# Kernel optimization log

Measured on AMD Instinct MI355X. Metric: run time of the kernel, lower is better.

The kernel has to match this reference:

```python
import jax, jax.numpy as jnp
import numpy as np

RADIUS = 4  # matches init radius


def _bilinear_sample(v, grid):
    """Faithful F.grid_sample(v, grid, mode='bilinear', align_corners=True, padding_mode='zeros').
    v: (B,C,H,W); grid: (B,Hg,Wg,2) in [-1,1]; grid[...,0]->width(x), grid[...,1]->height(y)."""
    B, C, H, W = v.shape
    Hg, Wg = grid.shape[1], grid.shape[2]
    ix = (grid[..., 0] + 1.0) * 0.5 * (W - 1)
    iy = (grid[..., 1] + 1.0) * 0.5 * (H - 1)
    x0 = jnp.floor(ix); y0 = jnp.floor(iy)
    x1 = x0 + 1.0;      y1 = y0 + 1.0
    wx1 = ix - x0; wx0 = 1.0 - wx1
    wy1 = iy - y0; wy0 = 1.0 - wy1
    v_flat = v.reshape(B, C, H * W)
    out = jnp.zeros((B, C, Hg, Wg), v.dtype)
    for xf, yf, w in ((x0, y0, wx0 * wy0), (x1, y0, wx1 * wy0),
                      (x0, y1, wx0 * wy1), (x1, y1, wx1 * wy1)):
        valid = (xf >= 0) & (xf <= W - 1) & (yf >= 0) & (yf <= H - 1)
        xi = jnp.clip(xf, 0, W - 1).astype(jnp.int32)
        yi = jnp.clip(yf, 0, H - 1).astype(jnp.int32)
        idx = (yi * W + xi).reshape(B, 1, Hg * Wg)
        g = jnp.take_along_axis(v_flat, idx, axis=2).reshape(B, C, Hg, Wg)
        out = out + g * (w * valid)[:, None, :, :]
    return out


def setup_inputs() -> dict:
    key = jax.random.key(0)
    ks = jax.random.split(key, 5)
    B, C, H, W, K = 4, 128, 128, 128, 8
    x = jax.random.normal(ks[0], (B, C, H, W), jnp.float32)
    psf_tbl = jax.random.randint(ks[1], (B, H, W, K, 2), 0, 128)  # absolute pixel anchors
    delta = jax.random.normal(ks[2], (1, 1, 1, K, 2), jnp.float32) * 0.1
    w_qkv = jax.random.normal(ks[3], (3 * C, C), jnp.float32) * (C ** -0.5)  # 1x1 conv, no bias
    w_proj = jax.random.normal(ks[4], (C, C), jnp.float32) * (C ** -0.5)
    return {"x": x, "psf_tbl": psf_tbl, "delta": delta, "w_qkv": w_qkv, "w_proj": w_proj}


def reference(x, psf_tbl, delta, w_qkv, w_proj):
    B, C, H, W = x.shape
    K = psf_tbl.shape[3]
    qkv = jnp.einsum('oc,bchw->bohw', w_qkv, x)  # 1x1 conv to_qkv
    q, k, v = jnp.split(qkv, 3, axis=1)
    offsets = psf_tbl.astype(x.dtype) + jnp.tanh(delta) * RADIUS  # (B,H,W,K,2)
    norm = jnp.array([H - 1, W - 1], x.dtype)
    grid = (offsets / norm * 2.0 - 1.0).reshape(B, H, W * K, 2)
    k_s = _bilinear_sample(k, grid).reshape(B, C, H, W, K)
    v_s = _bilinear_sample(v, grid).reshape(B, C, H, W, K)
    attn = jnp.einsum('bchw,bchwk->bhwk', q, k_s) * (C ** -0.5)
    attn = jax.nn.softmax(attn, axis=-1)  # softmax over K sampled points
    out = jnp.einsum('bhwk,bchwk->bchw', attn, v_s)
    return x + jnp.einsum('oc,bchw->bohw', w_proj, out)
```

## Files before the change

### kernel.cpp

```cpp
#include <hip/hip_runtime.h>

#define HW 16384
#define C 128

typedef __attribute__((ext_vector_type(8))) short short8;
typedef __attribute__((ext_vector_type(4))) float f32x4;
typedef __attribute__((ext_vector_type(2))) float f32x2;
typedef __attribute__((ext_vector_type(16))) int v16i;

__device__ __forceinline__ unsigned short f2bf(float f) {
  union { float f; unsigned u; } v; v.f = f;
  return (unsigned short)((v.u + 0x7fffu + ((v.u >> 16) & 1u)) >> 16);
}
#if __has_builtin(__builtin_amdgcn_cvt_pk_bf16_f32)
typedef __attribute__((ext_vector_type(2))) __bf16 bf16x2;
__device__ __forceinline__ unsigned pk2(float a, float b) {
  union { bf16x2 v; unsigned u; } cv;
  cv.v = __builtin_amdgcn_cvt_pk_bf16_f32(a, b);
  return cv.u;
}
#else
__device__ __forceinline__ unsigned pk2(float a, float b) {
  return (unsigned)f2bf(a) | ((unsigned)f2bf(b) << 16);
}
#endif
__device__ __forceinline__ unsigned short f2bf1(float a) {
  return (unsigned short)(pk2(a, a) & 0xffffu);
}
__device__ __forceinline__ float bflo(unsigned w) {
  union { unsigned u; float f; } v; v.u = w << 16; return v.f;
}
__device__ __forceinline__ float bfhi(unsigned w) {
  union { unsigned u; float f; } v; v.u = w & 0xffff0000u; return v.f;
}
__device__ __forceinline__ float asf(int u) {
  union { int u; float f; } v; v.u = u; return v.f;
}
__device__ __forceinline__ float bf2f(unsigned short h) {
  union { unsigned u; float f; } v; v.u = ((unsigned)h) << 16; return v.f;
}

__global__ __launch_bounds__(128) void k_prep(const float* __restrict__ w_qkv,
                                              const float* __restrict__ w_proj,
                                              const float* __restrict__ delta,
                                              unsigned short* __restrict__ Mt,
                                              unsigned short* __restrict__ Pm,
                                              float* __restrict__ pw,
                                              int* __restrict__ pi) {
  const int bid = blockIdx.x;
  const int t = threadIdx.x;
  if (bid == 256) {
    if (t < 8) {
      float s0 = tanhf(delta[t * 2 + 0]) * 4.0f;
      float s1 = tanhf(delta[t * 2 + 1]) * 4.0f;
      float f0 = floorf(s0), f1 = floorf(s1);
      pi[2 * t + 0] = (int)f0;
      pi[2 * t + 1] = (int)f1;
      float fx = s0 - f0, fy = s1 - f1;
      pw[4 * t + 0] = (1.0f - fx) * (1.0f - fy);
      pw[4 * t + 1] = fx * (1.0f - fy);
      pw[4 * t + 2] = (1.0f - fx) * fy;
      pw[4 * t + 3] = fx * fy;
    }
    return;
  }
  const int R = bid & 127;
  float acc = 0.0f;
  if (bid < 128) {
    const float* wq = w_qkv;
    const float* wk = w_qkv + 128 * 128;
    #pragma unroll 16
    for (int j = 0; j < 128; ++j)
      acc += wk[j * 128 + R] * wq[j * 128 + t];
    acc *= 0.08838834764831845f;
    Mt[R * 128 + (t ^ ((R & 7) << 3))] = f2bf1(acc);
  } else {
    const float* wv = w_qkv + 2 * 128 * 128;
    const float* wp = w_proj + (size_t)R * 128;
    #pragma unroll 16
    for (int j = 0; j < 128; ++j)
      acc += wp[j] * wv[j * 128 + t];
    Pm[R * 128 + (t ^ ((R & 7) << 3))] = f2bf1(acc);
  }
}

__global__ __launch_bounds__(256) void k_qx(const float* __restrict__ x,
                                            const unsigned short* __restrict__ Mt,
                                            unsigned short* __restrict__ qb,
                                            unsigned* __restrict__ xq) {
  __shared__ __align__(16) unsigned char smem[65536];
  unsigned short* Xs = (unsigned short*)smem;
  unsigned short* Ws = (unsigned short*)(smem + 32768);
  const int t = threadIdx.x;
  const int gpix0 = blockIdx.x * 128;
  const int b = gpix0 >> 14;
  const int hw0 = gpix0 & (HW - 1);

  const float* xb = x + (size_t)b * C * HW + hw0;
  #pragma unroll
  for (int i = 0; i < 16; ++i) {
    int linear = i * 256 + t;
    int p = linear & 127;
    int c4 = (linear >> 7) * 4;
    float a0 = xb[(size_t)(c4 + 0) * HW + p];
    float a1 = xb[(size_t)(c4 + 1) * HW + p];
    float a2 = xb[(size_t)(c4 + 2) * HW + p];
    float a3 = xb[(size_t)(c4 + 3) * HW + p];
    int cc = c4 ^ ((p & 7) << 3);
    *(uint2*)&Xs[p * 128 + cc] = make_uint2(pk2(a0, a1), pk2(a2, a3));
  }
  #pragma unroll
  for (int i = 0; i < 8; ++i)
    ((uint4*)Ws)[i * 256 + t] = ((const uint4*)Mt)[i * 256 + t];
  __syncthreads();

  #pragma unroll
  for (int i = 0; i < 8; ++i) {
    int linear = i * 256 + t;
    int c8 = (linear & 15) * 8;
    int prow = linear >> 4;
    uint4 v = *(const uint4*)&Xs[prow * 128 + (c8 ^ ((prow & 7) << 3))];
    *(uint4*)&xq[((size_t)(gpix0 + prow)) * 64 + (c8 >> 1)] = v;
  }

  const int wave = t >> 6, lane = t & 63;
  const int wr = wave >> 1, wc = wave & 1;
  const int rsel = lane & 15, quad = lane >> 4;

  f32x4 acc[4][4];
  #pragma unroll
  for (int mi = 0; mi < 4; ++mi)
    #pragma unroll
    for (int ni = 0; ni < 4; ++ni) acc[mi][ni] = (f32x4){0.f, 0.f, 0.f, 0.f};
  #pragma unroll
  for (int ks = 0; ks < 4; ++ks) {
    const int koff = ks * 32 + quad * 8;
    short8 afr[4], bfr[4];
    #pragma unroll
    for (int mi = 0; mi < 4; ++mi) {
      int r = wr * 64 + mi * 16 + rsel;
      afr[mi] = *(const short8*)&Xs[r * 128 + (koff ^ ((r & 7) << 3))];
    }
    #pragma unroll
    for (int ni = 0; ni < 4; ++ni) {
      int r = wc * 64 + ni * 16 + rsel;
      bfr[ni] = *(const short8*)&Ws[r * 128 + (koff ^ ((r & 7) << 3))];
    }
    #pragma unroll
    for (int mi = 0; mi < 4; ++mi)
      #pragma unroll
      for (int ni = 0; ni < 4; ++ni)
        acc[mi][ni] = __builtin_amdgcn_mfma_f32_16x16x32_bf16(afr[mi], bfr[ni], acc[mi][ni], 0, 0, 0);
  }
  __syncthreads();
  #pragma unroll
  for (int mi = 0; mi < 4; ++mi)
    #pragma unroll
    for (int ni = 0; ni < 4; ++ni)
      #pragma unroll
      for (int r = 0; r < 4; ++r) {
        int p = wr * 64 + mi * 16 + quad * 4 + r;
        int ch = wc * 64 + ni * 16 + rsel;
        Xs[p * 128 + (ch ^ ((p & 7) << 3))] = f2bf1(acc[mi][ni][r]);
      }
  __syncthreads();
  #pragma unroll
  for (int i = 0; i < 8; ++i) {
    int linear = i * 256 + t;
    int c8 = (linear & 15) * 8;
    int prow = linear >> 4;
    uint4 v = *(const uint4*)&Xs[prow * 128 + (c8 ^ ((prow & 7) << 3))];
    *(uint4*)(qb + (size_t)(gpix0 + prow) * C + c8) = v;
  }
}

__global__ __launch_bounds__(256) void k_attn(const unsigned short* __restrict__ qb,
                                              const unsigned* __restrict__ xq,
                                              const int* __restrict__ psf,
                                              const int* __restrict__ pwu,
                                              const int* __restrict__ pi,
                                              unsigned short* __restrict__ ao) {
  (void)pi;
  const int t = threadIdx.x;
  const int lane = t & 63;
  const int p = blockIdx.x;
  const int b = (p >> 1) & 3;
  const int j = ((p >> 3) << 1) | (p & 1);
  const int spix = __builtin_amdgcn_readfirstlane((b << 14) + (j << 2) + (t >> 6));

  const unsigned* xB = xq + (size_t)b * HW * 64;

  const unsigned qp = ((const unsigned*)qb)[(size_t)spix * 64 + lane];
  const float qx = bflo(qp), qy = bfhi(qp);

  v16i w0, w1, tpi, ps;
  asm volatile(
      "s_load_dwordx16 %0, %4, 0\n\t"
      "s_load_dwordx16 %1, %4, 64\n\t"
      "s_load_dwordx16 %2, %4, 128\n\t"
      "s_load_dwordx16 %3, %5, 0\n\t"
      "s_waitcnt lgkmcnt(0)"
      : "=&s"(w0), "=&s"(w1), "=&s"(tpi), "=&s"(ps)
      : "s"(pwu), "s"(psf + (size_t)spix * 16));

  unsigned wreg[32];
  #pragma unroll
  for (int k = 0; k < 8; ++k) {
    const int x0 = ps[k * 2 + 0] + tpi[2 * k + 0];
    const int y0 = ps[k * 2 + 1] + tpi[2 * k + 1];
    #pragma unroll
    for (int cn = 0; cn < 4; ++cn) {
      const int xc = min(max(x0 + (cn & 1), 0), 127);
      const int yc = min(max(y0 + (cn >> 1), 0), 127);
      wreg[k * 4 + cn] = xB[((size_t)((yc << 7) + xc) << 6) + lane];
    }
  }

  float dk[8];
  float2 xt[8];
  #pragma unroll
  for (int k = 0; k < 8; ++k) {
    const int x0 = ps[k * 2 + 0] + tpi[2 * k + 0];
    const int y0 = ps[k * 2 + 1] + tpi[2 * k + 1];
    float sx = 0.f, sy = 0.f;
    #pragma unroll
    for (int cn = 0; cn < 4; ++cn) {
      const int xi = x0 + (cn & 1);
      const int yi = y0 + (cn >> 1);
      const bool valid = (xi >= 0) & (xi <= 127) & (yi >= 0) & (yi <= 127);
      const int widx = k * 4 + cn;
      const int wbits = (widx < 16) ? w0[widx & 15] : w1[widx & 15];
      const float wv = asf(valid ? wbits : 0);
      const unsigned w = wreg[widx];
      sx = fmaf(bflo(w), wv, sx);
      sy = fmaf(bfhi(w), wv, sy);
    }
    xt[k] = make_float2(sx, sy);
    dk[k] = fmaf(qx, sx, qy * sy);
  }
  #pragma unroll
  for (int off = 32; off > 0; off >>= 1) {
    #pragma unroll
    for (int k = 0; k < 8; ++k) dk[k] += __shfl_xor(dk[k], off);
  }
  float m = dk[0];
  #pragma unroll
  for (int k = 1; k < 8; ++k) m = fmaxf(m, dk[k]);
  float den = 0.0f;
  #pragma unroll
  for (int k = 0; k < 8; ++k) { dk[k] = __expf(dk[k] - m); den += dk[k]; }
  const float inv = 1.0f / den;
  float ox = 0, oy = 0;
  #pragma unroll
  for (int k = 0; k < 8; ++k) { float pk = dk[k] * inv; ox += pk * xt[k].x; oy += pk * xt[k].y; }
  ((unsigned*)ao)[(size_t)spix * 64 + lane] = pk2(ox, oy);
}

__global__ __launch_bounds__(256) void k_proj(const unsigned short* __restrict__ ao,
                                              const unsigned short* __restrict__ Pm,
                                              const unsigned short* __restrict__ xqh,
                                              float* __restrict__ out) {
  __shared__ __align__(16) unsigned short As[128 * 128];
  __shared__ __align__(16) unsigned short Ws[128 * 128];
  const int t = threadIdx.x;
  const int gpix0 = blockIdx.x * 128;
  const int b = gpix0 >> 14;
  const int hw0 = gpix0 & (HW - 1);

  #pragma unroll
  for (int i = 0; i < 8; ++i) {
    int linear = i * 256 + t;
    int c8 = (linear & 15) * 8;
    int p = linear >> 4;
    uint4 v = *(const uint4*)(ao + (size_t)(gpix0 + p) * C + c8);
    *(uint4*)&As[p * 128 + (c8 ^ ((p & 7) << 3))] = v;
  }
  #pragma unroll
  for (int i = 0; i < 8; ++i)
    ((uint4*)Ws)[i * 256 + t] = ((const uint4*)Pm)[i * 256 + t];
  __syncthreads();

  const int wave = t >> 6, lane = t & 63;
  const int wr = wave >> 1, wc = wave & 1;
  const int rsel = lane & 15, quad = lane >> 4;

  f32x4 acc[4][4];
  #pragma unroll
  for (int mi = 0; mi < 4; ++mi)
    #pragma unroll
    for (int ni = 0; ni < 4; ++ni) acc[mi][ni] = (f32x4){0.f, 0.f, 0.f, 0.f};

  #pragma unroll
  for (int ks = 0; ks < 4; ++ks) {
    const int koff = ks * 32 + quad * 8;
    short8 afr[4], bfr[4];
    #pragma unroll
    for (int mi = 0; mi < 4; ++mi) {
      int r = wr * 64 + mi * 16 + rsel;
      afr[mi] = *(const short8*)&Ws[r * 128 + (koff ^ ((r & 7) << 3))];
    }
    #pragma unroll
    for (int ni = 0; ni < 4; ++ni) {
      int r = wc * 64 + ni * 16 + rsel;
      bfr[ni] = *(const short8*)&As[r * 128 + (koff ^ ((r & 7) << 3))];
    }
    #pragma unroll
    for (int mi = 0; mi < 4; ++mi)
      #pragma unroll
      for (int ni = 0; ni < 4; ++ni)
        acc[mi][ni] = __builtin_amdgcn_mfma_f32_16x16x32_bf16(afr[mi], bfr[ni], acc[mi][ni], 0, 0, 0);
  }

  __syncthreads();
  #pragma unroll
  for (int i = 0; i < 8; ++i) {
    int linear = i * 256 + t;
    int c8 = (linear & 15) * 8;
    int p = linear >> 4;
    uint4 v = *(const uint4*)(xqh + (size_t)(gpix0 + p) * C + c8);
    *(uint4*)&As[p * 128 + (c8 ^ ((p & 7) << 3))] = v;
  }
  __syncthreads();

  #pragma unroll
  for (int mi = 0; mi < 4; ++mi)
    #pragma unroll
    for (int ni = 0; ni < 4; ++ni)
      #pragma unroll
      for (int r = 0; r < 4; ++r) {
        int och = wr * 64 + mi * 16 + quad * 4 + r;
        int pixl = wc * 64 + ni * 16 + rsel;
        float xr = bf2f(As[pixl * 128 + (och ^ ((pixl & 7) << 3))]);
        size_t addr = ((size_t)b * C + och) * HW + hw0 + pixl;
        out[addr] = xr + acc[mi][ni][r];
      }
}

extern "C" void kernel_launch(void* const* d_in, const int* in_sizes, int n_in,
                              void* d_out, int out_size, void* d_ws, size_t ws_size,
                              hipStream_t stream) {
  const float* x      = (const float*)d_in[0];
  const int*   psf    = (const int*)d_in[1];
  const float* delta  = (const float*)d_in[2];
  const float* w_qkv  = (const float*)d_in[3];
  const float* w_proj = (const float*)d_in[4];
  float* out = (float*)d_out;

  const size_t N = (size_t)4 * HW * C;
  unsigned short* qb = (unsigned short*)d_ws;
  unsigned short* xq = qb + N;
  unsigned short* ao = xq + N;
  unsigned short* Mt = ao + N;
  unsigned short* Pm = Mt + 16384;
  float* pw = (float*)(Pm + 16384);
  int*   pi = (int*)(pw + 32);

  k_prep<<<dim3(257), 128, 0, stream>>>(w_qkv, w_proj, delta, Mt, Pm, pw, pi);
  k_qx<<<dim3(512), 256, 0, stream>>>(x, Mt, qb, (unsigned*)xq);
  k_attn<<<dim3(HW), 256, 0, stream>>>(qb, (const unsigned*)xq, psf, (const int*)pw, pi, ao);
  k_proj<<<dim3(512), 256, 0, stream>>>(ao, Pm, xq, out);
}
```

Measured before the change: 154.1 us.

## Process two pixels per wave in attention gather with 8-byte loads

The attention kernel now maps each pixel to 32 lanes instead of 64, so each lane handles four channels through uint2 loads and stores. The grid is halved and the pixel-to-block mapping changes. The per-pixel PSF anchors move from a scalar load to per-lane vector loads. The shuffle reduction drops one step. The aim is fewer, wider memory transactions and less per-pixel instruction overhead in this gather-bound kernel, at the cost of more registers per lane and possibly more diverse gather addresses within a wave.

```diff
diff --git a/kernel.cpp b/kernel.cpp
--- a/kernel.cpp
+++ b/kernel.cpp
@@ -178,68 +178,60 @@
                                               const unsigned* __restrict__ xq,
                                               const int* __restrict__ psf,
                                               const int* __restrict__ pwu,
-                                              const int* __restrict__ pi,
                                               unsigned short* __restrict__ ao) {
-  (void)pi;
   const int t = threadIdx.x;
-  const int lane = t & 63;
-  const int p = blockIdx.x;
-  const int b = (p >> 1) & 3;
-  const int j = ((p >> 3) << 1) | (p & 1);
-  const int spix = __builtin_amdgcn_readfirstlane((b << 14) + (j << 2) + (t >> 6));
-
-  const unsigned* xB = xq + (size_t)b * HW * 64;
-
-  const unsigned qp = ((const unsigned*)qb)[(size_t)spix * 64 + lane];
-  const float qx = bflo(qp), qy = bfhi(qp);
-
-  v16i w0, w1, tpi, ps;
+  const int li = t & 31;
+  const int half = (t >> 5) & 1;
+  const int gid = blockIdx.x;
+  const int b = gid & 3;
+  const int grp = gid >> 2;
+  const int pixl = (grp << 3) + ((t >> 6) << 1) + half;
+  const size_t spix = ((size_t)b << 14) + pixl;
+
+  v16i w0, w1, tpi;
   asm volatile(
-      "s_load_dwordx16 %0, %4, 0\n\t"
-      "s_load_dwordx16 %1, %4, 64\n\t"
-      "s_load_dwordx16 %2, %4, 128\n\t"
-      "s_load_dwordx16 %3, %5, 0\n\t"
+      "s_load_dwordx16 %0, %3, 0\n\t"
+      "s_load_dwordx16 %1, %3, 64\n\t"
+      "s_load_dwordx16 %2, %3, 128\n\t"
       "s_waitcnt lgkmcnt(0)"
-      : "=&s"(w0), "=&s"(w1), "=&s"(tpi), "=&s"(ps)
-      : "s"(pwu), "s"(psf + (size_t)spix * 16));
-
-  unsigned wreg[32];
+      : "=&s"(w0), "=&s"(w1), "=&s"(tpi)
+      : "s"(pwu));
+
+  const int4* pr = (const int4*)(psf + spix * 16);
+  int4 a0 = pr[0], a1 = pr[1], a2 = pr[2], a3 = pr[3];
+  int va[16] = {a0.x, a0.y, a0.z, a0.w, a1.x, a1.y, a1.z, a1.w,
+                a2.x, a2.y, a2.z, a2.w, a3.x, a3.y, a3.z, a3.w};
+
+  const uint2 qp = *(const uint2*)((const unsigned*)qb + spix * 64 + 2 * li);
+  const float q0 = bflo(qp.x), q1 = bfhi(qp.x);
+  const float q2 = bflo(qp.y), q3 = bfhi(qp.y);
+
+  const unsigned* xB = xq + (((size_t)b << 14) << 6);
+
+  float s0[8], s1[8], s2[8], s3[8], dk[8];
   #pragma unroll
   for (int k = 0; k < 8; ++k) {
-    const int x0 = ps[k * 2 + 0] + tpi[2 * k + 0];
-    const int y0 = ps[k * 2 + 1] + tpi[2 * k + 1];
-    #pragma unroll
-    for (int cn = 0; cn < 4; ++cn) {
-      const int xc = min(max(x0 + (cn & 1), 0), 127);
-      const int yc = min(max(y0 + (cn >> 1), 0), 127);
-      wreg[k * 4 + cn] = xB[((size_t)((yc << 7) + xc) << 6) + lane];
-    }
-  }
-
-  float dk[8];
-  float2 xt[8];
-  #pragma unroll
-  for (int k = 0; k < 8; ++k) {
-    const int x0 = ps[k * 2 + 0] + tpi[2 * k + 0];
-    const int y0 = ps[k * 2 + 1] + tpi[2 * k + 1];
-    float sx = 0.f, sy = 0.f;
+    const int x0 = va[2 * k + 0] + tpi[2 * k + 0];
+    const int y0 = va[2 * k + 1] + tpi[2 * k + 1];
+    float t0 = 0.f, t1 = 0.f, t2 = 0.f, t3 = 0.f;
     #pragma unroll
     for (int cn = 0; cn < 4; ++cn) {
       const int xi = x0 + (cn & 1);
       const int yi = y0 + (cn >> 1);
-      const bool valid = (xi >= 0) & (xi <= 127) & (yi >= 0) & (yi <= 127);
+      const bool valid = ((unsigned)xi <= 127u) & ((unsigned)yi <= 127u);
+      const int xc = min(max(xi, 0), 127);
+      const int yc = min(max(yi, 0), 127);
       const int widx = k * 4 + cn;
-      const int wbits = (widx < 16) ? w0[widx & 15] : w1[widx & 15];
-      const float wv = asf(valid ? wbits : 0);
-      const unsigned w = wreg[widx];
-      sx = fmaf(bflo(w), wv, sx);
-      sy = fmaf(bfhi(w), wv, sy);
-    }
-    xt[k] = make_float2(sx, sy);
-    dk[k] = fmaf(qx, sx, qy * sy);
-  }
-  #pragma unroll
-  for (int off = 32; off > 0; off >>= 1) {
+      const float wv = valid ? asf(widx < 16 ? w0[widx & 15] : w1[widx & 15]) : 0.0f;
+      const uint2 w2 = *(const uint2*)&xB[((size_t)((yc << 7) + xc) << 6) + 2 * li];
+      t0 = fmaf(bflo(w2.x), wv, t0); t1 = fmaf(bfhi(w2.x), wv, t1);
+      t2 = fmaf(bflo(w2.y), wv, t2); t3 = fmaf(bfhi(w2.y), wv, t3);
+    }
+    s0[k] = t0; s1[k] = t1; s2[k] = t2; s3[k] = t3;
+    dk[k] = fmaf(q0, t0, fmaf(q1, t1, fmaf(q2, t2, q3 * t3)));
+  }
+  #pragma unroll
+  for (int off = 16; off > 0; off >>= 1) {
     #pragma unroll
     for (int k = 0; k < 8; ++k) dk[k] += __shfl_xor(dk[k], off);
   }
@@ -250,10 +242,14 @@
   #pragma unroll
   for (int k = 0; k < 8; ++k) { dk[k] = __expf(dk[k] - m); den += dk[k]; }
   const float inv = 1.0f / den;
-  float ox = 0, oy = 0;
-  #pragma unroll
-  for (int k = 0; k < 8; ++k) { float pk = dk[k] * inv; ox += pk * xt[k].x; oy += pk * xt[k].y; }
-  ((unsigned*)ao)[(size_t)spix * 64 + lane] = pk2(ox, oy);
+  float o0 = 0.f, o1 = 0.f, o2 = 0.f, o3 = 0.f;
+  #pragma unroll
+  for (int k = 0; k < 8; ++k) {
+    const float pk = dk[k] * inv;
+    o0 = fmaf(pk, s0[k], o0); o1 = fmaf(pk, s1[k], o1);
+    o2 = fmaf(pk, s2[k], o2); o3 = fmaf(pk, s3[k], o3);
+  }
+  *(uint2*)((unsigned*)ao + spix * 64 + 2 * li) = make_uint2(pk2(o0, o1), pk2(o2, o3));
 }
 
 __global__ __launch_bounds__(256) void k_proj(const unsigned short* __restrict__ ao,
@@ -354,9 +350,10 @@
   unsigned short* Pm = Mt + 16384;
   float* pw = (float*)(Pm + 16384);
   int*   pi = (int*)(pw + 32);
+  (void)pi;
 
   k_prep<<<dim3(257), 128, 0, stream>>>(w_qkv, w_proj, delta, Mt, Pm, pw, pi);
   k_qx<<<dim3(512), 256, 0, stream>>>(x, Mt, qb, (unsigned*)xq);
-  k_attn<<<dim3(HW), 256, 0, stream>>>(qb, (const unsigned*)xq, psf, (const int*)pw, pi, ao);
+  k_attn<<<dim3(8192), 256, 0, stream>>>(qb, (const unsigned*)xq, psf, (const int*)pw, ao);
   k_proj<<<dim3(512), 256, 0, stream>>>(ao, Pm, xq, out);
 }
```

After: 148.0 us. 1.04x faster.
